# Optimization experiments

Measured on AMD Instinct MI355X. Metric: run time of the kernel, lower is better.

## Reference

```python
import jax, jax.numpy as jnp
import numpy as np

B, C, T, D = 256, 2, 25, 4096
H = 512          # LSTM units (num_features)
H1 = 128         # fc1 hidden
NC = 2           # num_classes
LEAKY_ALPHA = 0.2  # tf.nn.leaky_relu default


def setup_inputs() -> dict:
    key = jax.random.key(0)
    ks = jax.random.split(key, 8)
    return {
        "x": jax.random.normal(ks[0], (B, C, T, D), dtype=jnp.float32),
        "kernel": jax.random.normal(ks[1], (D, 4 * H), dtype=jnp.float32) * 0.02,
        "rec_kernel": jax.random.normal(ks[2], (H, 4 * H), dtype=jnp.float32) * 0.02,
        "bias": jax.random.normal(ks[3], (4 * H,), dtype=jnp.float32) * 0.02,
        "w1": jax.random.normal(ks[4], (H, H1), dtype=jnp.float32) * 0.05,
        "b1": jax.random.normal(ks[5], (H1,), dtype=jnp.float32) * 0.05,
        "w2": jax.random.normal(ks[6], (H1, NC), dtype=jnp.float32) * 0.05,
        "b2": jax.random.normal(ks[7], (NC,), dtype=jnp.float32) * 0.05,
    }


def _lstm(xc, kernel, rec_kernel, bias):
    # xc: [B, T, D]; Keras gate order i, f, c(g), o
    h = xc.shape[0], rec_kernel.shape[0]
    zx = jnp.einsum('btd,dg->btg', xc, kernel) + bias      # [B, T, 4H]
    zx_t = jnp.swapaxes(zx, 0, 1)                           # [T, B, 4H]
    nH = rec_kernel.shape[0]
    h0 = jnp.zeros((xc.shape[0], nH), dtype=xc.dtype)
    c0 = jnp.zeros((xc.shape[0], nH), dtype=xc.dtype)

    def step(carry, z_in):
        h, c = carry
        z = z_in + h @ rec_kernel                           # [B, 4H]
        i, f, g, o = jnp.split(z, 4, axis=-1)
        i = jax.nn.sigmoid(i)
        f = jax.nn.sigmoid(f)
        g = jnp.tanh(g)
        o = jax.nn.sigmoid(o)
        c = f * c + i * g
        h = o * jnp.tanh(c)
        return (h, c), None

    (hT, _), _ = jax.lax.scan(step, (h0, c0), zx_t)
    return hT                                               # [B, H]


def reference(x, kernel, rec_kernel, bias, w1, b1, w2, b2):
    xc = x[:, 0]                                            # rgb channel (ix=0)
    h = _lstm(xc, kernel, rec_kernel, bias)
    y = jax.nn.leaky_relu(h @ w1 + b1, negative_slope=LEAKY_ALPHA)
    # dropout inactive at inference (training=False)
    return jax.nn.softmax(y @ w2 + b2, axis=-1)             # [B, NC]
```

## Files before the change

kernel.cpp:

```cpp
#include <hip/hip_runtime.h>


typedef __bf16 bf16x8 __attribute__((ext_vector_type(8)));
typedef float  f32x4  __attribute__((ext_vector_type(4)));

#define MFMA16(a, b, c) __builtin_amdgcn_mfma_f32_16x16x32_bf16((a), (b), (c), 0, 0, 0)

__device__ __forceinline__ float sigmf(float x) {
  return 1.0f / (1.0f + __expf(-x));
}
__device__ __forceinline__ float tanhf_(float x) {
  float a = fabsf(x);
  float e = __expf(-2.0f * a);
  float r = (1.0f - e) / (1.0f + e);
  return copysignf(r, x);
}

__device__ __forceinline__ void async16(__bf16* lds, const __bf16* g) {
  __builtin_amdgcn_global_load_lds(
      (const __attribute__((address_space(1))) unsigned int*)g,
      (__attribute__((address_space(3))) unsigned int*)lds, 16, 0, 0);
}

__global__ __launch_bounds__(256) void conv_xb(const float* __restrict__ x,
                                               __bf16* __restrict__ xb) {
  long o = ((long)blockIdx.x * 256 + threadIdx.x) * 8;
  int m = (int)(o >> 12);
  int k = (int)(o & 4095);
  int b = m / 25, t = m - b * 25;
  const float* src = x + (long)b * 204800 + (long)t * 4096 + k;
  f32x4 v0 = *(const f32x4*)src;
  f32x4 v1 = *(const f32x4*)(src + 4);
  bf16x8 r;
  r[0] = (__bf16)v0[0]; r[1] = (__bf16)v0[1];
  r[2] = (__bf16)v0[2]; r[3] = (__bf16)v0[3];
  r[4] = (__bf16)v1[0]; r[5] = (__bf16)v1[1];
  r[6] = (__bf16)v1[2]; r[7] = (__bf16)v1[3];
  *(bf16x8*)(xb + o) = r;
}

__global__ __launch_bounds__(256) void conv_wkT(const float* __restrict__ wk,
                                                __bf16* __restrict__ wkT) {
  __shared__ float tile[64][65];
  const int k0 = blockIdx.y * 64;
  const int n0 = blockIdx.x * 64;
  const int tx = threadIdx.x & 63;
  const int ty = threadIdx.x >> 6;
#pragma unroll
  for (int p = 0; p < 16; ++p) {
    int kr = ty + p * 4;
    tile[kr][tx] = wk[(long)(k0 + kr) * 2048 + n0 + tx];
  }
  __syncthreads();
#pragma unroll
  for (int p = 0; p < 16; ++p) {
    int nr = ty + p * 4;
    wkT[(long)(n0 + nr) * 4096 + k0 + tx] = (__bf16)tile[tx][nr];
  }
}

__global__ __launch_bounds__(256) void conv_recF2(const float* __restrict__ rec,
                                                  __bf16* __restrict__ recF) {
  __shared__ float tile[512][17];
  const int tid = threadIdx.x;
  const int g  = blockIdx.x >> 5;
  const int jt = blockIdx.x & 31;
#pragma unroll 4
  for (int p = 0; p < 32; ++p) {
    int k = (p << 4) + (tid >> 4);
    tile[k][tid & 15] = rec[(long)k * 2048 + (g << 9) + (jt << 4) + (tid & 15)];
  }
  __syncthreads();
  const int l = tid & 63;
  const int w = tid >> 6;
  long obase = ((long)((g * 32 + jt) * 16)) * 512;
#pragma unroll
  for (int q = 0; q < 4; ++q) {
    int ks = (w << 2) + q;
    bf16x8 v;
#pragma unroll
    for (int i = 0; i < 8; ++i)
      v[i] = (__bf16)tile[(ks << 5) + ((l >> 4) << 3) + i][l & 15];
    *(bf16x8*)(recF + obase + (long)ks * 512 + l * 8) = v;
  }
}

__global__ __launch_bounds__(256) void gemm_bf16(const __bf16* __restrict__ A,
                                                 const __bf16* __restrict__ Bt,
                                                 const float* __restrict__ bias,
                                                 float* __restrict__ zx) {
  __shared__ __bf16 As[128 * 64];
  __shared__ __bf16 Bs[128 * 64];
  const int tid  = threadIdx.x;
  const int wid  = tid >> 6;
  const int lane = tid & 63;

  const int bid = blockIdx.x;
  const int swz = (bid & 7) * 100 + (bid >> 3);
  const int m0 = (swz >> 4) << 7;
  const int n0 = (swz & 15) << 7;

  const int srow  = (wid << 3) + (lane >> 3);
  const int skoff = (lane & 7) << 3;

  const int wr   = (wid >> 1) << 6;
  const int wc   = (wid & 1) << 6;
  const int lrow = lane & 15;
  const int lk8  = (lane >> 4) << 3;

  f32x4 acc[4][4];
#pragma unroll
  for (int i = 0; i < 4; ++i)
#pragma unroll
    for (int jj = 0; jj < 4; ++jj) {
      f32x4 z = {0.f, 0.f, 0.f, 0.f};
      acc[i][jj] = z;
    }

  const __bf16* Ag = A  + (long)(m0 + srow) * 4096 + skoff;
  const __bf16* Bg = Bt + (long)(n0 + srow) * 4096 + skoff;
  __bf16* Al = &As[(wid << 3) * 64];
  __bf16* Bl = &Bs[(wid << 3) * 64];

  for (int k0 = 0; k0 < 4096; k0 += 64) {
    __syncthreads();
#pragma unroll
    for (int q = 0; q < 4; ++q) {
      async16(Al + q * (32 * 64), Ag + (long)(q * 32) * 4096 + k0);
      async16(Bl + q * (32 * 64), Bg + (long)(q * 32) * 4096 + k0);
    }
    __syncthreads();
#pragma unroll
    for (int kk = 0; kk < 2; ++kk) {
      bf16x8 af[4], bv[4];
#pragma unroll
      for (int fr = 0; fr < 4; ++fr)
        af[fr] = *(const bf16x8*)&As[(wr + fr * 16 + lrow) * 64 + (kk << 5) + lk8];
#pragma unroll
      for (int fc = 0; fc < 4; ++fc)
        bv[fc] = *(const bf16x8*)&Bs[(wc + fc * 16 + lrow) * 64 + (kk << 5) + lk8];
#pragma unroll
      for (int fr = 0; fr < 4; ++fr)
#pragma unroll
        for (int fc = 0; fc < 4; ++fc)
          acc[fr][fc] = MFMA16(af[fr], bv[fc], acc[fr][fc]);
    }
  }

  const int mlow = (lane >> 4) << 2;
#pragma unroll
  for (int fc = 0; fc < 4; ++fc) {
    int n = n0 + wc + fc * 16 + lrow;
    float bvs = bias[n];
#pragma unroll
    for (int fr = 0; fr < 4; ++fr) {
      int mb = m0 + wr + fr * 16 + mlow;
#pragma unroll
      for (int r = 0; r < 4; ++r)
        zx[(long)(mb + r) * 2048 + n] = acc[fr][fc][r] + bvs;
    }
  }
}

__global__ __launch_bounds__(256) void lstm_persist(const float* __restrict__ zx,
                                                    const __bf16* __restrict__ recF,
                                                    __bf16* __restrict__ hA,
                                                    __bf16* __restrict__ hB,
                                                    __bf16* __restrict__ hplain,
                                                    int* bar) {
  __shared__ __bf16 recS[32768];
  const int tid  = threadIdx.x;
  const int wid  = tid >> 6;
  const int lane = tid & 63;
  const int bid  = blockIdx.x;
  const int jt   = bid & 31;
  const int rtg  = bid >> 5;
  const int rt   = (rtg << 2) + wid;
  int* gbar = bar + (rtg << 6);

  {
    const __bf16* src = recF + (long)(jt << 4) * 512;
#pragma unroll
    for (int g = 0; g < 4; ++g)
#pragma unroll
      for (int q = 0; q < 4; ++q)
        *(bf16x8*)(recS + g * 8192 + q * 2048 + tid * 8) =
            *(const bf16x8*)(src + (long)g * 262144 + q * 2048 + tid * 8);
  }

  const int j    = (jt << 4) + (lane & 15);
  const int mlow = (lane >> 4) << 2;
  const int ks2  = j >> 5;
  const int lhi  = ((j >> 3) & 3) << 4;
  const int i2   = j & 7;
  float c[4];
  int brow[4];
#pragma unroll
  for (int r = 0; r < 4; ++r) {
    c[r] = 0.f;
    brow[r] = (rt << 4) + mlow + r;
  }
  __syncthreads();

  float zv[4][4];
#pragma unroll
  for (int g = 0; g < 4; ++g)
#pragma unroll
    for (int r = 0; r < 4; ++r)
      zv[g][r] = zx[(((long)brow[r] * 25) << 11) + (g << 9) + j];

  const __bf16* hin = hA;
  __bf16* hout = hA;

  for (int t = 0; t < 25; ++t) {
    if (t > 0) {
      f32x4 acc[4];
#pragma unroll
      for (int g = 0; g < 4; ++g) {
        f32x4 z = {0.f, 0.f, 0.f, 0.f};
        acc[g] = z;
      }
#pragma unroll 4
      for (int ks = 0; ks < 16; ++ks) {
        bf16x8 a = *(const bf16x8*)(hin + ((((rt << 4) + ks) << 6) + lane) * 8);
#pragma unroll
        for (int g = 0; g < 4; ++g) {
          bf16x8 b = *(const bf16x8*)(recS + ((((g << 4) + ks) << 6) + lane) * 8);
          acc[g] = MFMA16(a, b, acc[g]);
        }
      }
#pragma unroll
      for (int g = 0; g < 4; ++g)
#pragma unroll
        for (int r = 0; r < 4; ++r)
          zv[g][r] += acc[g][r];
    }

#pragma unroll
    for (int r = 0; r < 4; ++r) {
      float ig = sigmf(zv[0][r]);
      float fg = sigmf(zv[1][r]);
      float gg = tanhf_(zv[2][r]);
      float og = sigmf(zv[3][r]);
      float cn = fg * c[r] + ig * gg;
      c[r] = cn;
      float hv = og * tanhf_(cn);
      hout[((((rt << 4) + ks2) << 6) + (lhi | (brow[r] & 15))) * 8 + i2] = (__bf16)hv;
      if (t == 24) hplain[(brow[r] << 9) + j] = (__bf16)hv;
    }

    if (t < 24) {
#pragma unroll
      for (int g = 0; g < 4; ++g)
#pragma unroll
        for (int r = 0; r < 4; ++r)
          zv[g][r] = zx[(((long)brow[r] * 25 + t + 1) << 11) + (g << 9) + j];

      __syncthreads();
      if (tid == 0)
        __hip_atomic_store(&gbar[jt], t + 1, __ATOMIC_RELEASE,
                           __HIP_MEMORY_SCOPE_AGENT);
      if (tid < 32) {
        while (__hip_atomic_load(&gbar[tid], __ATOMIC_ACQUIRE,
                                 __HIP_MEMORY_SCOPE_AGENT) < t + 1)
          __builtin_amdgcn_s_sleep(4);
      }
      __syncthreads();
    }

    hin  = hout;
    hout = (t & 1) ? hA : hB;
  }
}

__global__ __launch_bounds__(128) void head_kernel(const __bf16* __restrict__ h,
                                                   const float* __restrict__ w1,
                                                   const float* __restrict__ b1,
                                                   const float* __restrict__ w2,
                                                   const float* __restrict__ b2,
                                                   float* __restrict__ out) {
  const int b = blockIdx.x;
  const int j = threadIdx.x;
  float acc = b1[j];
#pragma unroll 8
  for (int k = 0; k < 512; ++k)
    acc += (float)h[b * 512 + k] * w1[k * 128 + j];
  float y = acc > 0.f ? acc : 0.2f * acc;

  __shared__ float s0[128], s1[128];
  s0[j] = y * w2[j * 2 + 0];
  s1[j] = y * w2[j * 2 + 1];
  __syncthreads();
#pragma unroll
  for (int s = 64; s > 0; s >>= 1) {
    if (j < s) { s0[j] += s0[j + s]; s1[j] += s1[j + s]; }
    __syncthreads();
  }
  if (j == 0) {
    float l0 = s0[0] + b2[0];
    float l1 = s1[0] + b2[1];
    float m  = fmaxf(l0, l1);
    float e0 = __expf(l0 - m);
    float e1 = __expf(l1 - m);
    float inv = 1.0f / (e0 + e1);
    out[b * 2 + 0] = e0 * inv;
    out[b * 2 + 1] = e1 * inv;
  }
}

extern "C" void kernel_launch(void* const* d_in, const int* in_sizes, int n_in,
                              void* d_out, int out_size, void* d_ws, size_t ws_size,
                              hipStream_t stream) {
  const float* x    = (const float*)d_in[0];
  const float* wk   = (const float*)d_in[1];
  const float* rec  = (const float*)d_in[2];
  const float* bias = (const float*)d_in[3];
  const float* w1   = (const float*)d_in[4];
  const float* b1   = (const float*)d_in[5];
  const float* w2   = (const float*)d_in[6];
  const float* b2   = (const float*)d_in[7];
  float* out = (float*)d_out;

  char* w = (char*)d_ws;
  float*  zx     = (float*)(w + 0);
  __bf16* xb     = (__bf16*)(w + 52428800);
  __bf16* wkT    = (__bf16*)(w + 104857600);
  __bf16* recF   = (__bf16*)(w + 121634816);
  __bf16* hA     = (__bf16*)(w + 123731968);
  __bf16* hB     = (__bf16*)(w + 123994112);
  __bf16* hplain = (__bf16*)(w + 124256256);
  int*    bar    = (int*)(w + 124518400);

  hipMemsetAsync(bar, 0, 1024, stream);

  conv_xb   <<<12800, 256, 0, stream>>>(x, xb);
  conv_wkT  <<<dim3(32, 64), 256, 0, stream>>>(wk, wkT);
  conv_recF2<<<128, 256, 0, stream>>>(rec, recF);

  gemm_bf16<<<800, 256, 0, stream>>>(xb, wkT, bias, zx);

  lstm_persist<<<128, 256, 0, stream>>>(zx, recF, hA, hB, hplain, bar);

  head_kernel<<<256, 128, 0, stream>>>(hplain, w1, b1, w2, b2, out);
}
```

Before: 736.5 us.

## Repartition persistent LSTM into 8 barrier groups of 16 blocks with 32-column tiles

The persistent LSTM kernel now splits the batch into 8 groups of 32 rows, each served by 16 blocks that each own 32 hidden columns and hold twice the recurrent weights in LDS. This halves the number of blocks each grid barrier must wait on, cutting synchronisation latency per timestep. The barrier store is moved before the next-step zx prefetch, and polling now uses relaxed loads followed by a single acquire load. The GEMM also drops its swizzled block mapping for a plain 2D grid, which may hurt L2 locality.

```diff
diff --git a/kernel.cpp b/kernel.cpp
--- a/kernel.cpp
+++ b/kernel.cpp
@@ -94,11 +94,8 @@
   const int tid  = threadIdx.x;
   const int wid  = tid >> 6;
   const int lane = tid & 63;
-
-  const int bid = blockIdx.x;
-  const int swz = (bid & 7) * 100 + (bid >> 3);
-  const int m0 = (swz >> 4) << 7;
-  const int n0 = (swz & 15) << 7;
+  const int m0 = blockIdx.y * 128;
+  const int n0 = blockIdx.x * 128;
 
   const int srow  = (wid << 3) + (lane >> 3);
   const int skoff = (lane & 7) << 3;
@@ -168,37 +165,43 @@
                                                     __bf16* __restrict__ hB,
                                                     __bf16* __restrict__ hplain,
                                                     int* bar) {
-  __shared__ __bf16 recS[32768];
+  __shared__ __bf16 recS[65536];
   const int tid  = threadIdx.x;
   const int wid  = tid >> 6;
   const int lane = tid & 63;
   const int bid  = blockIdx.x;
-  const int jt   = bid & 31;
-  const int rtg  = bid >> 5;
-  const int rt   = (rtg << 2) + wid;
-  int* gbar = bar + (rtg << 6);
+  const int g8   = bid & 7;
+  const int jb   = bid >> 3;
+  const int rt   = wid >> 1;
+  const int jt2  = wid & 1;
+  const int rtile = (g8 << 1) + rt;
+  int* gbar = bar + (g8 << 6);
 
   {
-    const __bf16* src = recF + (long)(jt << 4) * 512;
 #pragma unroll
     for (int g = 0; g < 4; ++g)
 #pragma unroll
-      for (int q = 0; q < 4; ++q)
-        *(bf16x8*)(recS + g * 8192 + q * 2048 + tid * 8) =
-            *(const bf16x8*)(src + (long)g * 262144 + q * 2048 + tid * 8);
-  }
-
-  const int j    = (jt << 4) + (lane & 15);
-  const int mlow = (lane >> 4) << 2;
-  const int ks2  = j >> 5;
-  const int lhi  = ((j >> 3) & 3) << 4;
+      for (int c2 = 0; c2 < 2; ++c2) {
+        const __bf16* src = recF + ((long)(g * 32 + (jb << 1) + c2) << 13);
+        __bf16* dst = recS + (((g << 1) + c2) << 13);
+#pragma unroll
+        for (int q = 0; q < 4; ++q)
+          *(bf16x8*)(dst + (q << 11) + tid * 8) =
+              *(const bf16x8*)(src + (q << 11) + tid * 8);
+      }
+  }
+
+  const int lrow = lane & 15;
+  const int lhi4 = lane >> 4;
+  const int j    = (jb << 5) + (jt2 << 4) + lrow;
+  const int khi  = (j >> 3) & 3;
   const int i2   = j & 7;
   float c[4];
   int brow[4];
 #pragma unroll
   for (int r = 0; r < 4; ++r) {
     c[r] = 0.f;
-    brow[r] = (rt << 4) + mlow + r;
+    brow[r] = (g8 << 5) + (rt << 4) + (lhi4 << 2) + r;
   }
   __syncthreads();
 
@@ -222,10 +225,11 @@
       }
 #pragma unroll 4
       for (int ks = 0; ks < 16; ++ks) {
-        bf16x8 a = *(const bf16x8*)(hin + ((((rt << 4) + ks) << 6) + lane) * 8);
+        bf16x8 a = *(const bf16x8*)(hin + ((((rtile << 4) + ks) << 6) + lane) * 8);
 #pragma unroll
         for (int g = 0; g < 4; ++g) {
-          bf16x8 b = *(const bf16x8*)(recS + ((((g << 4) + ks) << 6) + lane) * 8);
+          bf16x8 b = *(const bf16x8*)(recS +
+              (((((g << 1) + jt2) << 4) + ks) << 9) + lane * 8);
           acc[g] = MFMA16(a, b, acc[g]);
         }
       }
@@ -245,25 +249,29 @@
       float cn = fg * c[r] + ig * gg;
       c[r] = cn;
       float hv = og * tanhf_(cn);
-      hout[((((rt << 4) + ks2) << 6) + (lhi | (brow[r] & 15))) * 8 + i2] = (__bf16)hv;
+      int lane_w = (khi << 4) | (lhi4 << 2) | r;
+      hout[((((rtile << 4) + jb) << 6) + lane_w) * 8 + i2] = (__bf16)hv;
       if (t == 24) hplain[(brow[r] << 9) + j] = (__bf16)hv;
     }
 
     if (t < 24) {
+      __syncthreads();
+      if (tid == 0)
+        __hip_atomic_store(&gbar[jb], t + 1, __ATOMIC_RELEASE,
+                           __HIP_MEMORY_SCOPE_AGENT);
+
 #pragma unroll
       for (int g = 0; g < 4; ++g)
 #pragma unroll
         for (int r = 0; r < 4; ++r)
           zv[g][r] = zx[(((long)brow[r] * 25 + t + 1) << 11) + (g << 9) + j];
 
-      __syncthreads();
-      if (tid == 0)
-        __hip_atomic_store(&gbar[jt], t + 1, __ATOMIC_RELEASE,
-                           __HIP_MEMORY_SCOPE_AGENT);
-      if (tid < 32) {
-        while (__hip_atomic_load(&gbar[tid], __ATOMIC_ACQUIRE,
+      if (tid < 16) {
+        while (__hip_atomic_load(&gbar[tid], __ATOMIC_RELAXED,
                                  __HIP_MEMORY_SCOPE_AGENT) < t + 1)
-          __builtin_amdgcn_s_sleep(4);
+          __builtin_amdgcn_s_sleep(2);
+        (void)__hip_atomic_load(&gbar[tid], __ATOMIC_ACQUIRE,
+                                __HIP_MEMORY_SCOPE_AGENT);
       }
       __syncthreads();
     }
@@ -331,13 +339,13 @@
   __bf16* hplain = (__bf16*)(w + 124256256);
   int*    bar    = (int*)(w + 124518400);
 
-  hipMemsetAsync(bar, 0, 1024, stream);
+  hipMemsetAsync(bar, 0, 2048, stream);
 
   conv_xb   <<<12800, 256, 0, stream>>>(x, xb);
   conv_wkT  <<<dim3(32, 64), 256, 0, stream>>>(wk, wkT);
   conv_recF2<<<128, 256, 0, stream>>>(rec, recF);
 
-  gemm_bf16<<<800, 256, 0, stream>>>(xb, wkT, bias, zx);
+  gemm_bf16<<<dim3(16, 50), 256, 0, stream>>>(xb, wkT, bias, zx);
 
   lstm_persist<<<128, 256, 0, stream>>>(zx, recF, hA, hB, hplain, bar);
 
```

Result: faster. 705.4 us (-4.2%).
